# Performance work log

Hardware: AMD Instinct MI355X
Metric: run time of the kernel (lower is better)

## Reference

```python
import jax, jax.numpy as jnp
import numpy as np

# model dims
B, L, D, K = 4, 1024, 512, 24      # batch, seq_len, d_model, num_eigh
KU, KY, NL, DT = 3, 2, 4, 512      # ar depth u, ar depth y, num_layers, d_target
EPS = 1e-5


def _hankel_eigh():
    # Hankel matrix Z[i,j] = 2 / ((i+j)^3 - (i+j)), i,j in 1..L; top-K eigenpairs
    idx = np.arange(1, L + 1, dtype=np.float64)
    s = idx[:, None] + idx[None, :]
    Z = 2.0 / (s ** 3 - s)
    vals, vecs = np.linalg.eigh(Z)  # ascending
    return (jnp.asarray(vals[-K:], jnp.float32),       # [K]
            jnp.asarray(vecs[:, -K:], jnp.float32))    # [L, K]


def setup_inputs() -> dict:
    key = jax.random.key(0)
    ks = jax.random.split(key, 12)
    sc = 1.0 / np.sqrt(D)
    eig_vals, eig_vecs = _hankel_eigh()
    return {
        "inputs": jax.random.normal(ks[0], (B, L, D), jnp.float32),
        "emb_w": jax.random.normal(ks[1], (D, D), jnp.float32) * sc,
        "emb_b": jnp.zeros((D,), jnp.float32),
        "ln_scale": jnp.ones((NL, D), jnp.float32),
        "ln_bias": jnp.zeros((NL, D), jnp.float32),
        "m_y": jax.random.normal(ks[2], (NL, D, KY, D), jnp.float32) * 0.02,
        "m_u": jax.random.normal(ks[3], (NL, D, D, KU), jnp.float32) * sc,
        "m_phi": jax.random.normal(ks[4], (NL, D * K, D), jnp.float32) * 0.02,
        "w1": jax.random.normal(ks[5], (NL, D, 2 * D), jnp.float32) * sc,
        "b1": jnp.zeros((NL, 2 * D), jnp.float32),
        "proj_w": jax.random.normal(ks[6], (D, DT), jnp.float32) * sc,
        "proj_b": jnp.zeros((DT,), jnp.float32),
        "eig_vals": eig_vals,
        "eig_vecs": eig_vecs,
    }


def _layer_norm(x, s, b):
    mu = jnp.mean(x, axis=-1, keepdims=True)
    var = jnp.mean(jnp.square(x - mu), axis=-1, keepdims=True)
    return (x - mu) * jax.lax.rsqrt(var + EPS) * s + b


def _stu(x, m_y_l, m_u_l, m_phi_l, eig_vals, eig_vecs):
    # x: [B, L, D]
    n = 2 * L
    U = jnp.fft.rfft(x, n=n, axis=1)                 # [B, nf, D]
    V = jnp.fft.rfft(eig_vecs, n=n, axis=0)          # [nf, K]
    # causal conv of each eigvec filter with each channel -> x_tilde [B, L, K, D]
    xt = jnp.fft.irfft(U[:, :, None, :] * V[None, :, :, None], n=n, axis=1)[:, :L]
    xt = xt * (eig_vals[None, None, :, None] ** 0.25)
    delta_phi = xt.reshape(B, L, K * D) @ m_phi_l    # [B, L, D]
    ar = jnp.zeros_like(delta_phi)
    for i in range(KU):
        c = jnp.einsum('bli,oi->blo', x, m_u_l[:, :, i])
        if i > 0:
            c = jnp.pad(c, ((0, 0), (i, 0), (0, 0)))[:, :L]
        ar = ar + c
    deltas = delta_phi + ar
    # y_t = sum_{j<KY} m_y[:,j,:] @ y_{t-1-j} + delta_t  (sequential recurrence)
    def step(carry, d_t):                            # carry [B, KY, D], d_t [B, D]
        y = jnp.einsum('okd,bkd->bo', m_y_l, carry) + d_t
        carry = jnp.concatenate([y[:, None, :], carry[:, :-1]], axis=1)
        return carry, y
    _, ys = jax.lax.scan(step, jnp.zeros((B, KY, D), x.dtype),
                         jnp.transpose(deltas, (1, 0, 2)))
    return jnp.transpose(ys, (1, 0, 2))              # [B, L, D]


def reference(inputs, emb_w, emb_b, ln_scale, ln_bias, m_y, m_u, m_phi,
              w1, b1, proj_w, proj_b, eig_vals, eig_vecs):
    x = inputs @ emb_w + emb_b
    for l in range(NL):
        z = x
        h = _layer_norm(x, ln_scale[l], ln_bias[l])
        h = _stu(h, m_y[l], m_u[l], m_phi[l], eig_vals, eig_vecs)
        h = jax.nn.gelu(h, approximate=False)        # torch GELU default (erf)
        g = h @ w1[l] + b1[l]
        a, b = jnp.split(g, 2, axis=-1)
        h = a * jax.nn.sigmoid(b)                    # GLU(dim=-1)
        x = h + z                                    # residual (dropout=0, eval)
    return x @ proj_w + proj_b
```

## Files before the change

### kernel.cpp

```cpp
#include <hip/hip_runtime.h>
#include <math.h>

typedef __bf16 bf;
typedef __attribute__((ext_vector_type(4))) __bf16 bfv4;
typedef __attribute__((ext_vector_type(8))) __bf16 bfv8;
typedef __attribute__((ext_vector_type(4))) float f32x4;

__device__ __forceinline__ void gload16(const void* g, void* l) {
  __builtin_amdgcn_global_load_lds((const __attribute__((address_space(1))) void*)g,
                                   (__attribute__((address_space(3))) void*)l, 16, 0, 0);
}

struct GOp {
  const bf* A; long la, lKa, lMa, sAz; int zshA, kzA;
  const bf* B; long lb, lKb, sBz; int zmskB, kzB;
  float* C; long ldc, sCz;
  bf* Cb; long ldcb, sCbz;
  const float* bias; int K, maskCmp, mBlk;
};

template<int tB,int tF32,int tB16,int tMASK,int tACC>
__device__ __forceinline__ void gbody(const GOp g, int z, bf* lsA, bf* lsB, const bf* zpg) {
  const int t = threadIdx.x;
  const long m0 = (long)blockIdx.x * 128, n0 = (long)blockIdx.y * 128;
  const bf* Ap = g.A + (long)(z >> g.zshA) * g.sAz;
  const bf* Bp = g.B + (long)(z & g.zmskB) * g.sBz;
  const int w = t >> 6, l = t & 63;
  const int wm = (w >> 1) * 64, wn = (w & 1) * 64;
  const int lr = l & 15, lk = (l >> 4) * 8;
  const int r0 = t >> 2, ko = (t & 3) * 8;
  const long rowA1 = m0 + r0, rowA2 = rowA1 + 64;
  const long baseA1 = (rowA1 >> 9) * g.lMa + (rowA1 & 511) * g.la;
  const long baseA2 = (rowA2 >> 9) * g.lMa + (rowA2 & 511) * g.la;
  const long baseB1 = (n0 + r0) * g.lb;
  const int zbA = z * g.kzA, zbB = z * g.kzB;
  const int ct = ((int)rowA1 + 1) & 7;
  const long convB = (long)ct * 2065 + 1023 - (long)rowA1;
  f32x4 acc[4][4];
  #pragma unroll
  for (int i = 0; i < 4; i++)
    #pragma unroll
    for (int j = 0; j < 4; j++) acc[i][j] = (f32x4){0.f, 0.f, 0.f, 0.f};

  for (int k0 = 0; k0 < g.K; k0 += 32) {
    const int kk = k0 + ko;
    const int bA = (kk >> 9) + zbA, bB = (kk >> 9) + zbB;
    const long kb = (long)bB * g.lKb + (kk & 511);
    const bf* ga; const bf* ga2;
    if (tMASK == 3) {
      ga  = Ap + convB + kk;
      ga2 = ga - 64;
    } else {
      const long ka = (long)bA * g.lKa + (kk & 511);
      ga  = Ap + baseA1 + ka;
      ga2 = Ap + baseA2 + ka;
      if (tMASK == 1) { if ((int)(rowA1 & 15) < bA) { ga = zpg; ga2 = zpg; } }
      if (tMASK == 2) { if ((int)(rowA1 & 63) < g.maskCmp) { ga = zpg; ga2 = zpg; } }
    }
    const bf* gb = Bp + baseB1 + kb;
    gload16(ga,            &lsA[t * 8]);
    gload16(ga2,           &lsA[2048 + t * 8]);
    gload16(gb,            &lsB[t * 8]);
    gload16(gb + 64 * g.lb, &lsB[2048 + t * 8]);
    __syncthreads();
    bfv8 av[4], bv[4];
    #pragma unroll
    for (int i = 0; i < 4; i++) av[i] = *(const bfv8*)&lsA[(wm + i * 16 + lr) * 32 + lk];
    #pragma unroll
    for (int i = 0; i < 4; i++) bv[i] = *(const bfv8*)&lsB[(wn + i * 16 + lr) * 32 + lk];
    #pragma unroll
    for (int i = 0; i < 4; i++)
      #pragma unroll
      for (int j = 0; j < 4; j++)
        acc[i][j] = __builtin_amdgcn_mfma_f32_16x16x32_bf16(av[i], bv[j], acc[i][j], 0, 0, 0);
    __syncthreads();
  }
  const int orow = (l >> 4) * 4, ocol = lr;
  #pragma unroll
  for (int i = 0; i < 4; i++)
    #pragma unroll
    for (int j = 0; j < 4; j++) {
      long col = n0 + wn + j * 16 + ocol;
      float bb = tB ? g.bias[col] : 0.f;
      #pragma unroll
      for (int r = 0; r < 4; r++) {
        long row = m0 + wm + i * 16 + orow + r;
        float v = acc[i][j][r] + bb;
        if (tF32) {
          long idx = (long)z * g.sCz + row * g.ldc + col;
          if (tACC) v += g.C[idx];
          g.C[idx] = v;
        }
        if (tB16) g.Cb[(long)z * g.sCbz + row * g.ldcb + col] = (bf)v;
      }
    }
}

template<int tB,int tF32,int tB16,int tMASK,int tACC,int tSPEC,
         int sB,int sF32,int sB16,int sMASK,int sACC>
__global__ __launch_bounds__(256) void gemm_k(GOp g, GOp gx, const bf* __restrict__ zpg) {
  __shared__ bf lsA[4096], lsB[4096];
  int z = blockIdx.z;
  if (tSPEC && z == (int)gridDim.z - 1) {
    if ((int)blockIdx.x >= gx.mBlk) return;
    gbody<sB,sF32,sB16,sMASK,sACC>(gx, 0, lsA, lsB, zpg);
  } else {
    gbody<tB,tF32,tB16,tMASK,tACC>(g, z, lsA, lsB, zpg);
  }
}

static inline GOp mkop(const void* A, long la, long lKa, long lMa, long sAz, int zshA, int kzA,
                       const void* B, long lb, long lKb, long sBz, int zmskB, int kzB,
                       void* C, long ldc, long sCz, void* Cb, long ldcb, long sCbz,
                       const void* bias, int K, int maskCmp, int mBlk) {
  GOp g;
  g.A = (const bf*)A; g.la = la; g.lKa = lKa; g.lMa = lMa; g.sAz = sAz; g.zshA = zshA; g.kzA = kzA;
  g.B = (const bf*)B; g.lb = lb; g.lKb = lKb; g.sBz = sBz; g.zmskB = zmskB; g.kzB = kzB;
  g.C = (float*)C; g.ldc = ldc; g.sCz = sCz;
  g.Cb = (bf*)Cb; g.ldcb = ldcb; g.sCbz = sCbz;
  g.bias = (const float*)bias; g.K = K; g.maskCmp = maskCmp; g.mBlk = mBlk;
  return g;
}

template<int tB,int tF32,int tB16,int tMASK,int tACC,int tSPEC=0,
         int sB=0,int sF32=0,int sB16=0,int sMASK=0,int sACC=0>
static inline void LG(hipStream_t st, int gx, int gy, int gz, const GOp& g, const GOp& gs, const bf* zpg) {
  gemm_k<tB,tF32,tB16,tMASK,tACC,tSPEC,sB,sF32,sB16,sMASK,sACC>
      <<<dim3(gx, gy, gz), 256, 0, st>>>(g, gs, zpg);
}


template<typename TI, typename TO>
__global__ __launch_bounds__(256) void k_trt(const TI* __restrict__ in, TO* __restrict__ out,
                                             long ldin, long inz, long ldout, long outz) {
  __shared__ float tile[64][65];
  int z = blockIdx.z;
  int c0 = blockIdx.x * 64, r0 = blockIdx.y * 64;
  int tx = threadIdx.x & 63, ty = threadIdx.x >> 6;
  #pragma unroll
  for (int i = ty; i < 64; i += 4) tile[i][tx] = (float)in[(long)z * inz + (long)(c0 + i) * ldin + r0 + tx];
  __syncthreads();
  #pragma unroll
  for (int i = ty; i < 64; i += 4) out[(long)z * outz + (long)(r0 + i) * ldout + c0 + tx] = (TO)tile[tx][i];
}

__global__ __launch_bounds__(256) void k_trtS(const float* __restrict__ in, bf* __restrict__ out,
                                              long ldin, long ldout, const float* __restrict__ scl) {
  __shared__ float tile[64][65];
  int c0 = blockIdx.x * 64, r0 = blockIdx.y * 64;
  int tx = threadIdx.x & 63, ty = threadIdx.x >> 6;
  #pragma unroll
  for (int i = ty; i < 64; i += 4) tile[i][tx] = in[(long)(c0 + i) * ldin + r0 + tx];
  __syncthreads();
  float sc = scl[(c0 + tx) >> 9];
  #pragma unroll
  for (int i = ty; i < 64; i += 4) out[(long)(r0 + i) * ldout + c0 + tx] = (bf)(tile[tx][i] * sc);
}

__global__ void k_scl(const float* __restrict__ evals, float* __restrict__ scl) {
  int k = threadIdx.x;
  if (k < 24) scl[k] = powf(evals[k], 0.25f);
}

__global__ void k_pvec(const float* __restrict__ evecs, bf* __restrict__ out) {
  long id = (long)blockIdx.x * 256 + threadIdx.x;
  if (id >= 24L * 16512) return;
  int kf = (int)(id / 16512);
  int rem = (int)(id % 16512);
  int c = rem / 2064, j = rem % 2064;
  int d = j - c;
  float v = (d >= 0 && d <= 1023) ? evecs[(long)(1023 - d) * 24 + kf] : 0.f;
  out[id] = (bf)v;
}

__global__ void k_mut(const float* __restrict__ mul_, bf* __restrict__ out) {
  long id = (long)blockIdx.x * 256 + threadIdx.x;
  long r = id >> 9; int d = (int)(id & 511);
  int i = (int)(r >> 9), o = (int)(r & 511);
  out[id] = (bf)mul_[(long)o * 1536 + d * 3 + i];
}

__global__ void k_buildCM(const float* __restrict__ myl, bf* __restrict__ cmpow) {
  long id = (long)blockIdx.x * 256 + threadIdx.x;
  int half = (int)(id >> 20);
  int r = (int)(id & 1048575);
  int p = r >> 10, q = r & 1023;
  float v;
  if (half == 0) v = (p == q) ? 1.f : 0.f;
  else if (p < 512) v = myl[(long)p * 1024 + q];
  else v = (q == p - 512) ? 1.f : 0.f;
  cmpow[id] = (bf)v;
}

__global__ __launch_bounds__(256) void k_ln(const float* __restrict__ x, const float* __restrict__ sc,
                                            const float* __restrict__ bi, bf* __restrict__ hb) {
  __shared__ float red[8];
  long row = blockIdx.x;
  const float* xr = x + row * 512;
  int t = threadIdx.x;
  float a = xr[t], b2 = xr[t + 256];
  float s = a + b2;
  #pragma unroll
  for (int o = 32; o; o >>= 1) s += __shfl_down(s, o, 64);
  if ((t & 63) == 0) red[t >> 6] = s;
  __syncthreads();
  float mu = (red[0] + red[1] + red[2] + red[3]) * (1.f / 512.f);
  __syncthreads();
  float c1 = a - mu, c2 = b2 - mu;
  float qq = c1 * c1 + c2 * c2;
  #pragma unroll
  for (int o = 32; o; o >>= 1) qq += __shfl_down(qq, o, 64);
  if ((t & 63) == 0) red[t >> 6] = qq;
  __syncthreads();
  float var = (red[0] + red[1] + red[2] + red[3]) * (1.f / 512.f);
  float rs = rsqrtf(var + 1e-5f);
  hb[row * 512 + t]       = (bf)(c1 * rs * sc[t] + bi[t]);
  hb[row * 512 + t + 256] = (bf)(c2 * rs * sc[t + 256] + bi[t + 256]);
}

__global__ void k_deltasS(const float* __restrict__ dp, long stride, int S,
                          const bf* __restrict__ callb, bf* __restrict__ db) {
  long id = (long)blockIdx.x * 256 + threadIdx.x;
  int o = (int)(id & 511); long row = id >> 9; int tt = (int)(row & 1023);
  float v = 0.f;
  for (int zz = 0; zz < S; ++zz) v += dp[(long)zz * stride + id];
  for (int i = 0; i < 3; ++i)
    if (tt >= i) v += (float)callb[(row - i) * 1536 + i * 512 + o];
  db[id] = (bf)v;
}

__global__ void k_egather(const float* __restrict__ dp, long stride, int S,
                          float* __restrict__ E, bf* __restrict__ eb0) {
  long id = (long)blockIdx.x * 256 + threadIdx.x;
  int p = (int)(id & 1023); long r = id >> 10;
  int b = (int)(r >> 6), c = (int)(r & 63);
  int tq = c * 16 + ((p < 512) ? 15 : 14);
  long idx = ((long)(b << 10) + tq) * 512 + (p & 511);
  float v = 0.f;
  for (int zz = 0; zz < S; ++zz) v += dp[(long)zz * stride + idx];
  E[id] = v; eb0[id] = (bf)v;
}

__global__ void k_sfinal(const float* __restrict__ E, bf* __restrict__ ssb) {
  long id = (long)blockIdx.x * 256 + threadIdx.x;
  int c = (int)((id >> 10) & 63);
  ssb[id] = (c > 0) ? (bf)E[id - 1024] : (bf)0.f;
}

__global__ void k_combgelu(const float* __restrict__ dp, long stride, int S,
                           const bf* __restrict__ outh, bf* __restrict__ yg) {
  long id = (long)blockIdx.x * 256 + threadIdx.x;
  int o = (int)(id & 511); long row = id >> 9;
  int b = (int)(row >> 10), tt = (int)(row & 1023);
  int c = tt >> 4, j = tt & 15;
  long wv = ((long)(j * 512 + o)) * 256 + b * 64 + c;
  float v = (float)outh[wv];
  for (int zz = 0; zz < S; ++zz) v += dp[(long)zz * stride + id];
  yg[id] = (bf)(0.5f * v * (1.f + erff(v * 0.70710678118654752f)));
}

__global__ void k_glures(const bf* __restrict__ g, float* __restrict__ x) {
  long id = (long)blockIdx.x * 256 + threadIdx.x;
  int o = (int)(id & 511); long row = id >> 9;
  float a = (float)g[row * 1024 + o], bb = (float)g[row * 1024 + 512 + o];
  x[id] = x[id] + a / (1.f + expf(-bb));
}

__global__ void k_cast(const float* __restrict__ in, bf* __restrict__ out, long n4) {
  long id = (long)blockIdx.x * 256 + threadIdx.x;
  if (id >= n4) return;
  float4 v = *(const float4*)(in + id * 4);
  bfv4 o; o[0] = (bf)v.x; o[1] = (bf)v.y; o[2] = (bf)v.z; o[3] = (bf)v.w;
  *(bfv4*)(out + id * 4) = o;
}

__global__ void k_fill(float* p, long n, float v) {
  long id = (long)blockIdx.x * 256 + threadIdx.x;
  if (id < n) p[id] = v;
}

struct Lay {
  long ZPG, SCL, EMBT, PROJT, PVEC, CMPOW, CMT2, WU, X, MPHITL, MUTL, W1TL,
       HB, HTB, DSLOT, DP, RC, E, EB0, EB1, SSTB, need;
  int nk, S;
};
static Lay mkLay(int nk, int S) {
  Lay L; long o = 0;
  auto al = [&](long sz) { long r = o; o += (sz + 255) & ~255L; return r; };
  L.nk = nk; L.S = S;
  L.ZPG   = al(4096);
  L.SCL   = al(256);
  L.EMBT  = al(524288);
  L.PROJT = al(524288);
  L.PVEC  = al(24L * 16512 * 2);
  L.CMPOW = al(17L * 2097152);
  L.CMT2  = al(2L * 2097152);
  L.WU    = al(8388608);
  L.X     = al(8388608);
  L.MPHITL= al(12582912);
  L.MUTL  = al(1572864);
  L.W1TL  = al(1048576);
  L.HB    = al(4194304);
  L.HTB   = al(4194304);
  L.DSLOT = al(4194304);
  L.DP    = al((long)S * 8388608);
  long rc = (long)nk * 4194304;
  if (rc < 16777216) rc = 16777216;
  L.RC    = al(rc);
  L.E     = al(1048576);
  L.EB0   = al(524288);
  L.EB1   = al(524288);
  L.SSTB  = al(524288);
  L.need  = o;
  return L;
}

extern "C" void kernel_launch(void* const* d_in, const int* in_sizes, int n_in,
                              void* d_out, int out_size, void* d_ws, size_t ws_size,
                              hipStream_t stream) {
  Lay L = mkLay(12, 4);
  if (L.need > (long)ws_size) L = mkLay(8, 4);
  if (L.need > (long)ws_size) L = mkLay(4, 2);
  if (L.need > (long)ws_size) {
    k_fill<<<8192, 256, 0, stream>>>((float*)d_out, 2097152, 1.0e6f + (float)(ws_size >> 20));
    return;
  }
  const float* inp  = (const float*)d_in[0];
  const float* embw = (const float*)d_in[1];
  const float* embb = (const float*)d_in[2];
  const float* lns  = (const float*)d_in[3];
  const float* lnb  = (const float*)d_in[4];
  const float* m_y  = (const float*)d_in[5];
  const float* m_u  = (const float*)d_in[6];
  const float* mphi = (const float*)d_in[7];
  const float* w1   = (const float*)d_in[8];
  const float* b1   = (const float*)d_in[9];
  const float* pw   = (const float*)d_in[10];
  const float* pb   = (const float*)d_in[11];
  const float* evals = (const float*)d_in[12];
  const float* evecs = (const float*)d_in[13];

  char* w = (char*)d_ws;
  bf*    ZPG   = (bf*)(w + L.ZPG);
  float* SCL   = (float*)(w + L.SCL);
  bf*    EMBT  = (bf*)(w + L.EMBT);
  bf*    PROJT = (bf*)(w + L.PROJT);
  bf*    PVEC  = (bf*)(w + L.PVEC);
  bf*    CMPOW = (bf*)(w + L.CMPOW);
  bf*    CMT2a = (bf*)(w + L.CMT2);
  bf*    CMT2b = CMT2a + 1048576;
  bf*    WUa   = (bf*)(w + L.WU);
  bf*    WUb   = (bf*)(w + L.WU + 4194304);
  float* X     = (float*)(w + L.X);
  bf*    MPHITL= (bf*)(w + L.MPHITL);
  bf*    MUTL  = (bf*)(w + L.MUTL);
  bf*    W1TL  = (bf*)(w + L.W1TL);
  bf*    HB    = (bf*)(w + L.HB);
  bf*    HTB   = (bf*)(w + L.HTB);
  bf*    DELTAB= (bf*)(w + L.DSLOT);
  bf*    YGB   = (bf*)(w + L.DSLOT);
  float* DP    = (float*)(w + L.DP);
  bf*    XTC   = (bf*)(w + L.RC);
  bf*    CALLB = (bf*)(w + L.RC);
  bf*    OUTH  = (bf*)(w + L.RC + 12582912);
  bf*    G     = (bf*)(w + L.RC);
  float* E     = (float*)(w + L.E);
  bf*    EB0   = (bf*)(w + L.EB0);
  bf*    EB1   = (bf*)(w + L.EB1);
  bf*    SSTB  = (bf*)(w + L.SSTB);
  bf*    INB   = HB;
  hipStream_t st = stream;
  const int nk = L.nk, S = L.S, nchunk = 24 / nk;
  const long DPS = 2097152;
  const int Kcphi = nk * 512 / S, kzphi = Kcphi >> 9;
  const int Kcy = 8192 / S, kzy = Kcy >> 9;
  GOp gnull = {};

  hipMemsetAsync(w + L.ZPG, 0, 4096, st);

  k_scl<<<1, 32, 0, st>>>(evals, SCL);
  k_pvec<<<1549, 256, 0, st>>>(evecs, PVEC);
  k_trt<float, bf><<<dim3(8, 8, 1), 256, 0, st>>>(embw, EMBT, 512, 0, 512, 0);
  k_trt<float, bf><<<dim3(8, 8, 1), 256, 0, st>>>(pw, PROJT, 512, 0, 512, 0);
  k_cast<<<2048, 256, 0, st>>>(inp, INB, 524288);
  LG<1,1,0,0,0>(st, 32, 4, 1,
      mkop(INB, 512, 512, 262144, 0, 30, 0, EMBT, 512, 512, 0, 0, 0,
           X, 512, 0, nullptr, 0, 0, embb, 512, 0, 0), gnull, ZPG);

  for (int l = 0; l < 4; ++l) {
    k_buildCM<<<8192, 256, 0, st>>>(m_y + (long)l * 524288, CMPOW);
    k_trt<bf, bf><<<dim3(16, 16, 1), 256, 0, st>>>(CMPOW + 1048576, CMT2a, 1024, 0, 1024, 0);
    bf* curT = CMT2a;
    for (int r = 0; r < 4; ++r) {
      int s = 1 << r;
      bf* nxtT = (r & 1) ? CMT2a : CMT2b;
      GOp mn = mkop(CMPOW + 1048576, 1024, 512, 524288, 1048576, 0, 0,
                    curT, 1024, 512, 0, 0, 0,
                    nullptr, 0, 0, CMPOW + (long)(s + 1) * 1048576, 1024, 1048576,
                    nullptr, 1024, 0, 0);
      GOp sp = mkop(curT, 1024, 512, 524288, 0, 30, 0,
                    CMPOW + (long)s * 1048576, 1024, 512, 0, 0, 0,
                    nullptr, 0, 0, nxtT, 1024, 0,
                    nullptr, 1024, 0, 8);
      LG<0,0,1,0,0, 1, 0,0,1,0,0>(st, 8, 8, s + 1, mn, sp, ZPG);
      curT = nxtT;
    }
    k_trtS<<<dim3(192, 8, 1), 256, 0, st>>>(mphi + (long)l * 6291456, MPHITL, 512, 12288, SCL);
    k_mut<<<3072, 256, 0, st>>>(m_u + (long)l * 786432, MUTL);
    k_trt<float, bf><<<dim3(8, 16, 1), 256, 0, st>>>(w1 + (long)l * 524288, W1TL, 1024, 0, 512, 0);

    k_ln<<<4096, 256, 0, st>>>(X, lns + l * 512, lnb + l * 512, HB);
    k_trt<bf, bf><<<dim3(16, 8, 4), 256, 0, st>>>(HB, HTB, 512, 524288, 1024, 524288);

    for (int kc = 0; kc < nchunk; ++kc) {
      LG<0,0,1,3,0>(st, 8, 4, 4 * nk,
          mkop(PVEC + (long)kc * nk * 16512, 0, 0, 0, 16512, 2, 0,
               HTB, 1024, 512, 524288, 3, 0,
               nullptr, 0, 0, XTC, 512, 524288, nullptr, 1024, 0, 0), gnull, ZPG);
      GOp pg = mkop(XTC, 512, 2097152, 262144, 0, 30, kzphi,
                    MPHITL + (long)kc * nk * 512, 12288, 512, 0, 0, kzphi,
                    DP, 512, DPS, nullptr, 0, 0, nullptr, Kcphi, 0, 0);
      if (kc == 0) LG<0,1,0,0,0>(st, 32, 4, S, pg, gnull, ZPG);
      else         LG<0,1,0,0,1>(st, 32, 4, S, pg, gnull, ZPG);
    }

    LG<0,0,1,0,0>(st, 32, 12, 1,
        mkop(HB, 512, 512, 262144, 0, 30, 0, MUTL, 512, 512, 0, 0, 0,
             nullptr, 0, 0, CALLB, 1536, 0, nullptr, 512, 0, 0), gnull, ZPG);
    k_deltasS<<<8192, 256, 0, st>>>(DP, DPS, S, CALLB, DELTAB);

    LG<0,1,0,1,0>(st, 32, 4, S,
        mkop(DELTAB, 512, -512, 262144, 0, 30, kzy,
             CMPOW, 1024, 1048576, 0, 0, kzy,
             DP, 512, DPS, nullptr, 0, 0, nullptr, Kcy, 0, 0), gnull, ZPG);

    k_egather<<<1024, 256, 0, st>>>(DP, DPS, S, E, EB0);
    const bf* Wc = CMPOW + 16L * 1048576;
    const bf* Uc = curT;
    bf* EBc = EB0; bf* EBn = EB1;
    bf* WUn = WUa;
    for (int k = 1; k <= 5; ++k) {
      int sh = 1 << (k - 1);
      GOp mn = mkop(Wc, 1024, 512, 524288, (long)(Uc - Wc), 0, 0,
                    Uc, 1024, 512, (long)(Wc - Uc), 1, 0,
                    nullptr, 0, 0, WUn, 1024, 1048576, nullptr, 1024, 0, 0);
      GOp sp = mkop(EBc - (long)sh * 1024, 1024, 512, 524288, 0, 30, 0,
                    Wc, 1024, 512, 0, 0, 0,
                    E, 1024, 0, EBn, 1024, 0, nullptr, 1024, sh, 2);
      LG<0,0,1,0,0, 1, 0,1,1,2,1>(st, 8, 8, 3, mn, sp, ZPG);
      Wc = WUn; Uc = WUn + 1048576;
      WUn = (k & 1) ? WUb : WUa;
      bf* tmp = EBc; EBc = EBn; EBn = tmp;
    }
    LG<0,1,0,2,1>(st, 2, 8, 1,
        mkop(EBc - 32L * 1024, 1024, 512, 524288, 0, 30, 0,
             Wc, 1024, 512, 0, 0, 0,
             E, 1024, 0, nullptr, 0, 0, nullptr, 1024, 32, 0), gnull, ZPG);
    k_sfinal<<<1024, 256, 0, st>>>(E, SSTB);

    LG<0,0,1,0,0>(st, 64, 2, 1,
        mkop(CMPOW + 1048576, 1024, 512, 1048576, 0, 30, 0,
             SSTB, 1024, 512, 0, 0, 0,
             nullptr, 0, 0, OUTH, 256, 0, nullptr, 1024, 0, 0), gnull, ZPG);
    k_combgelu<<<8192, 256, 0, st>>>(DP, DPS, S, OUTH, YGB);
    LG<1,0,1,0,0>(st, 32, 8, 1,
        mkop(YGB, 512, 512, 262144, 0, 30, 0, W1TL, 512, 512, 0, 0, 0,
             nullptr, 0, 0, G, 1024, 0, b1 + (long)l * 1024, 512, 0, 0), gnull, ZPG);
    k_glures<<<8192, 256, 0, st>>>(G, X);
  }

  k_cast<<<2048, 256, 0, st>>>(X, INB, 524288);
  LG<1,1,0,0,0>(st, 32, 4, 1,
      mkop(INB, 512, 512, 262144, 0, 30, 0, PROJT, 512, 512, 0, 0, 0,
           (float*)d_out, 512, 0, nullptr, 0, 0, pb, 512, 0, 0), gnull, ZPG);
}
```

Baseline: 3.136 ms.

## Fold companion-matrix power rounds into conv and phi GEMM launches as extra blocks

The four repeated-squaring rounds that build the powers of the AR-y companion matrix no longer run as standalone launches. Each round is appended as extra z-slices to a convolution or phi GEMM launch in the first chunk iterations, with the tile work flattened across blocks and split between a power-product op and a transpose-update op. The initial matrix build and its transpose are merged into one prep kernel that also writes the identity half of the transposed buffer. The aim is to cut launch count and fill idle compute units behind the small power GEMMs. The risk is that the power rounds now depend on enough chunk iterations existing, and that the extra blocks can lengthen the tail of the host GEMMs.

```diff
diff --git a/kernel.cpp b/kernel.cpp
--- a/kernel.cpp
+++ b/kernel.cpp
@@ -16,13 +16,13 @@
   const bf* B; long lb, lKb, sBz; int zmskB, kzB;
   float* C; long ldc, sCz;
   bf* Cb; long ldcb, sCbz;
-  const float* bias; int K, maskCmp, mBlk;
+  const float* bias; int K, maskCmp, mBlk, spS;
 };
 
 template<int tB,int tF32,int tB16,int tMASK,int tACC>
-__device__ __forceinline__ void gbody(const GOp g, int z, bf* lsA, bf* lsB, const bf* zpg) {
+__device__ __forceinline__ void gbody(const GOp g, int z, long m0, long n0,
+                                      bf* lsA, bf* lsB, const bf* zpg) {
   const int t = threadIdx.x;
-  const long m0 = (long)blockIdx.x * 128, n0 = (long)blockIdx.y * 128;
   const bf* Ap = g.A + (long)(z >> g.zshA) * g.sAz;
   const bf* Bp = g.B + (long)(z & g.zmskB) * g.sBz;
   const int w = t >> 6, l = t & 63;
@@ -58,9 +58,9 @@
       if (tMASK == 2) { if ((int)(rowA1 & 63) < g.maskCmp) { ga = zpg; ga2 = zpg; } }
     }
     const bf* gb = Bp + baseB1 + kb;
-    gload16(ga,            &lsA[t * 8]);
-    gload16(ga2,           &lsA[2048 + t * 8]);
-    gload16(gb,            &lsB[t * 8]);
+    gload16(ga,             &lsA[t * 8]);
+    gload16(ga2,            &lsA[2048 + t * 8]);
+    gload16(gb,             &lsB[t * 8]);
     gload16(gb + 64 * g.lb, &lsB[2048 + t * 8]);
     __syncthreads();
     bfv8 av[4], bv[4];
@@ -96,37 +96,45 @@
     }
 }
 
-template<int tB,int tF32,int tB16,int tMASK,int tACC,int tSPEC,
-         int sB,int sF32,int sB16,int sMASK,int sACC>
-__global__ __launch_bounds__(256) void gemm_k(GOp g, GOp gx, const bf* __restrict__ zpg) {
+template<int tB,int tF32,int tB16,int tMASK,int tACC,int tSPEC=0,
+         int sB=0,int sF32=0,int sB16=0,int sMASK=0,int sACC=0>
+__global__ __launch_bounds__(256) void gemm_k(GOp g, GOp gx, GOp gy, int Zmain,
+                                              const bf* __restrict__ zpg) {
   __shared__ bf lsA[4096], lsB[4096];
   int z = blockIdx.z;
-  if (tSPEC && z == (int)gridDim.z - 1) {
-    if ((int)blockIdx.x >= gx.mBlk) return;
-    gbody<sB,sF32,sB16,sMASK,sACC>(gx, 0, lsA, lsB, zpg);
+  if (tSPEC && z >= Zmain) {
+    int flat = (z - Zmain) * (int)(gridDim.x * gridDim.y)
+             + (int)blockIdx.y * (int)gridDim.x + (int)blockIdx.x;
+    if (flat >= gx.mBlk) return;
+    int zz = flat >> 6, t64 = flat & 63;
+    long m0 = (long)(t64 >> 3) * 128, n0 = (long)(t64 & 7) * 128;
+    if (zz < gx.spS) gbody<sB,sF32,sB16,sMASK,sACC>(gx, zz, m0, n0, lsA, lsB, zpg);
+    else             gbody<sB,sF32,sB16,sMASK,sACC>(gy, 0,  m0, n0, lsA, lsB, zpg);
   } else {
-    gbody<tB,tF32,tB16,tMASK,tACC>(g, z, lsA, lsB, zpg);
+    gbody<tB,tF32,tB16,tMASK,tACC>(g, z, (long)blockIdx.x * 128, (long)blockIdx.y * 128,
+                                   lsA, lsB, zpg);
   }
 }
 
 static inline GOp mkop(const void* A, long la, long lKa, long lMa, long sAz, int zshA, int kzA,
                        const void* B, long lb, long lKb, long sBz, int zmskB, int kzB,
                        void* C, long ldc, long sCz, void* Cb, long ldcb, long sCbz,
-                       const void* bias, int K, int maskCmp, int mBlk) {
+                       const void* bias, int K) {
   GOp g;
   g.A = (const bf*)A; g.la = la; g.lKa = lKa; g.lMa = lMa; g.sAz = sAz; g.zshA = zshA; g.kzA = kzA;
   g.B = (const bf*)B; g.lb = lb; g.lKb = lKb; g.sBz = sBz; g.zmskB = zmskB; g.kzB = kzB;
   g.C = (float*)C; g.ldc = ldc; g.sCz = sCz;
   g.Cb = (bf*)Cb; g.ldcb = ldcb; g.sCbz = sCbz;
-  g.bias = (const float*)bias; g.K = K; g.maskCmp = maskCmp; g.mBlk = mBlk;
+  g.bias = (const float*)bias; g.K = K; g.maskCmp = 0; g.mBlk = 0; g.spS = 0;
   return g;
 }
 
 template<int tB,int tF32,int tB16,int tMASK,int tACC,int tSPEC=0,
          int sB=0,int sF32=0,int sB16=0,int sMASK=0,int sACC=0>
-static inline void LG(hipStream_t st, int gx, int gy, int gz, const GOp& g, const GOp& gs, const bf* zpg) {
+static inline void LG(hipStream_t st, int gx_, int gy_, int gz_, const GOp& g,
+                      const GOp& gsx, const GOp& gsy, int Zmain, const bf* zpg) {
   gemm_k<tB,tF32,tB16,tMASK,tACC,tSPEC,sB,sF32,sB16,sMASK,sACC>
-      <<<dim3(gx, gy, gz), 256, 0, st>>>(g, gs, zpg);
+      <<<dim3(gx_, gy_, gz_), 256, 0, st>>>(g, gsx, gsy, Zmain, zpg);
 }
 
 
@@ -180,16 +188,38 @@
   out[id] = (bf)mul_[(long)o * 1536 + d * 3 + i];
 }
 
-__global__ void k_buildCM(const float* __restrict__ myl, bf* __restrict__ cmpow) {
-  long id = (long)blockIdx.x * 256 + threadIdx.x;
-  int half = (int)(id >> 20);
-  int r = (int)(id & 1048575);
-  int p = r >> 10, q = r & 1023;
-  float v;
-  if (half == 0) v = (p == q) ? 1.f : 0.f;
-  else if (p < 512) v = myl[(long)p * 1024 + q];
-  else v = (q == p - 512) ? 1.f : 0.f;
-  cmpow[id] = (bf)v;
+__global__ __launch_bounds__(256) void k_prep(const float* __restrict__ myl,
+                                              bf* __restrict__ cmpow, bf* __restrict__ trs) {
+  __shared__ float t[64][65];
+  long bid = blockIdx.x;
+  if (bid < 10240) {
+    long id = bid * 256 + threadIdx.x;
+    if (id < 2097152) {
+      int half = (int)(id >> 20);
+      int r = (int)(id & 1048575);
+      int p = r >> 10, q = r & 1023;
+      float v;
+      if (half == 0) v = (p == q) ? 1.f : 0.f;
+      else if (p < 512) v = myl[(long)p * 1024 + q];
+      else v = (q == p - 512) ? 1.f : 0.f;
+      cmpow[id] = (bf)v;
+    } else if (id < 2621440) {
+      long id2 = id - 2097152;
+      int x = (int)(id2 >> 9), y = (int)(id2 & 511);
+      trs[(long)x * 1024 + 512 + y] = (bf)((x == y) ? 1.f : 0.f);
+    }
+  } else {
+    int tile = (int)(bid - 10240);
+    int txx = tile >> 3, tyy = tile & 7;
+    int lx = threadIdx.x & 63, ly = threadIdx.x >> 6;
+    #pragma unroll
+    for (int i = ly; i < 64; i += 4)
+      t[i][lx] = myl[(long)(tyy * 64 + i) * 1024 + txx * 64 + lx];
+    __syncthreads();
+    #pragma unroll
+    for (int i = ly; i < 64; i += 4)
+      trs[(long)(txx * 64 + i) * 1024 + tyy * 64 + lx] = (bf)t[lx][i];
+  }
 }
 
 __global__ __launch_bounds__(256) void k_ln(const float* __restrict__ x, const float* __restrict__ sc,
@@ -280,8 +310,8 @@
 }
 
 struct Lay {
-  long ZPG, SCL, EMBT, PROJT, PVEC, CMPOW, CMT2, WU, X, MPHITL, MUTL, W1TL,
-       HB, HTB, DSLOT, DP, RC, E, EB0, EB1, SSTB, need;
+  long ZPG, SSTB, SCL, EMBT, PROJT, PVEC, CMPOW, TRS, WU, X, MPHITL, MUTL, W1TL,
+       HB, HTB, DSLOT, DP, RC, E, EB0, EB1, need;
   int nk, S;
 };
 static Lay mkLay(int nk, int S) {
@@ -289,12 +319,13 @@
   auto al = [&](long sz) { long r = o; o += (sz + 255) & ~255L; return r; };
   L.nk = nk; L.S = S;
   L.ZPG   = al(4096);
+  L.SSTB  = al(524288);
   L.SCL   = al(256);
   L.EMBT  = al(524288);
   L.PROJT = al(524288);
   L.PVEC  = al(24L * 16512 * 2);
   L.CMPOW = al(17L * 2097152);
-  L.CMT2  = al(2L * 2097152);
+  L.TRS   = al(2L * 2097152);
   L.WU    = al(8388608);
   L.X     = al(8388608);
   L.MPHITL= al(12582912);
@@ -310,7 +341,6 @@
   L.E     = al(1048576);
   L.EB0   = al(524288);
   L.EB1   = al(524288);
-  L.SSTB  = al(524288);
   L.need  = o;
   return L;
 }
@@ -342,13 +372,14 @@
 
   char* w = (char*)d_ws;
   bf*    ZPG   = (bf*)(w + L.ZPG);
+  bf*    SSTB  = (bf*)(w + L.SSTB);
   float* SCL   = (float*)(w + L.SCL);
   bf*    EMBT  = (bf*)(w + L.EMBT);
   bf*    PROJT = (bf*)(w + L.PROJT);
   bf*    PVEC  = (bf*)(w + L.PVEC);
   bf*    CMPOW = (bf*)(w + L.CMPOW);
-  bf*    CMT2a = (bf*)(w + L.CMT2);
-  bf*    CMT2b = CMT2a + 1048576;
+  bf*    TRSa  = (bf*)(w + L.TRS);
+  bf*    TRSb  = TRSa + 1048576;
   bf*    WUa   = (bf*)(w + L.WU);
   bf*    WUb   = (bf*)(w + L.WU + 4194304);
   float* X     = (float*)(w + L.X);
@@ -367,7 +398,6 @@
   float* E     = (float*)(w + L.E);
   bf*    EB0   = (bf*)(w + L.EB0);
   bf*    EB1   = (bf*)(w + L.EB1);
-  bf*    SSTB  = (bf*)(w + L.SSTB);
   bf*    INB   = HB;
   hipStream_t st = stream;
   const int nk = L.nk, S = L.S, nchunk = 24 / nk;
@@ -375,6 +405,7 @@
   const int Kcphi = nk * 512 / S, kzphi = Kcphi >> 9;
   const int Kcy = 8192 / S, kzy = Kcy >> 9;
   GOp gnull = {};
+  const int BIGZ = 1 << 30;
 
   hipMemsetAsync(w + L.ZPG, 0, 4096, st);
 
@@ -385,26 +416,10 @@
   k_cast<<<2048, 256, 0, st>>>(inp, INB, 524288);
   LG<1,1,0,0,0>(st, 32, 4, 1,
       mkop(INB, 512, 512, 262144, 0, 30, 0, EMBT, 512, 512, 0, 0, 0,
-           X, 512, 0, nullptr, 0, 0, embb, 512, 0, 0), gnull, ZPG);
+           X, 512, 0, nullptr, 0, 0, embb, 512), gnull, gnull, BIGZ, ZPG);
 
   for (int l = 0; l < 4; ++l) {
-    k_buildCM<<<8192, 256, 0, st>>>(m_y + (long)l * 524288, CMPOW);
-    k_trt<bf, bf><<<dim3(16, 16, 1), 256, 0, st>>>(CMPOW + 1048576, CMT2a, 1024, 0, 1024, 0);
-    bf* curT = CMT2a;
-    for (int r = 0; r < 4; ++r) {
-      int s = 1 << r;
-      bf* nxtT = (r & 1) ? CMT2a : CMT2b;
-      GOp mn = mkop(CMPOW + 1048576, 1024, 512, 524288, 1048576, 0, 0,
-                    curT, 1024, 512, 0, 0, 0,
-                    nullptr, 0, 0, CMPOW + (long)(s + 1) * 1048576, 1024, 1048576,
-                    nullptr, 1024, 0, 0);
-      GOp sp = mkop(curT, 1024, 512, 524288, 0, 30, 0,
-                    CMPOW + (long)s * 1048576, 1024, 512, 0, 0, 0,
-                    nullptr, 0, 0, nxtT, 1024, 0,
-                    nullptr, 1024, 0, 8);
-      LG<0,0,1,0,0, 1, 0,0,1,0,0>(st, 8, 8, s + 1, mn, sp, ZPG);
-      curT = nxtT;
-    }
+    k_prep<<<10368, 256, 0, st>>>(m_y + (long)l * 524288, CMPOW, TRSa);
     k_trtS<<<dim3(192, 8, 1), 256, 0, st>>>(mphi + (long)l * 6291456, MPHITL, 512, 12288, SCL);
     k_mut<<<3072, 256, 0, st>>>(m_u + (long)l * 786432, MUTL);
     k_trt<float, bf><<<dim3(8, 16, 1), 256, 0, st>>>(w1 + (long)l * 524288, W1TL, 1024, 0, 512, 0);
@@ -412,65 +427,103 @@
     k_ln<<<4096, 256, 0, st>>>(X, lns + l * 512, lnb + l * 512, HB);
     k_trt<bf, bf><<<dim3(16, 8, 4), 256, 0, st>>>(HB, HTB, 512, 524288, 1024, 524288);
 
+    int hostRound = 0;
     for (int kc = 0; kc < nchunk; ++kc) {
-      LG<0,0,1,3,0>(st, 8, 4, 4 * nk,
-          mkop(PVEC + (long)kc * nk * 16512, 0, 0, 0, 16512, 2, 0,
-               HTB, 1024, 512, 524288, 3, 0,
-               nullptr, 0, 0, XTC, 512, 524288, nullptr, 1024, 0, 0), gnull, ZPG);
-      GOp pg = mkop(XTC, 512, 2097152, 262144, 0, 30, kzphi,
-                    MPHITL + (long)kc * nk * 512, 12288, 512, 0, 0, kzphi,
-                    DP, 512, DPS, nullptr, 0, 0, nullptr, Kcphi, 0, 0);
-      if (kc == 0) LG<0,1,0,0,0>(st, 32, 4, S, pg, gnull, ZPG);
-      else         LG<0,1,0,0,1>(st, 32, 4, S, pg, gnull, ZPG);
+      GOp gconv = mkop(PVEC + (long)kc * nk * 16512, 0, 0, 0, 16512, 2, 0,
+                       HTB, 1024, 512, 524288, 3, 0,
+                       nullptr, 0, 0, XTC, 512, 524288, nullptr, 1024);
+      if (hostRound < 4) {
+        int s = 1 << hostRound;
+        bf* TRScur = (hostRound & 1) ? TRSb : TRSa;
+        bf* TRSnxt = (hostRound & 1) ? TRSa : TRSb;
+        GOp dx = mkop(CMPOW + 1048576, 1024, 512, 524288, 1048576, 0, 0,
+                      TRScur, 1024, 512, 0, 0, 0,
+                      nullptr, 0, 0, CMPOW + (long)(s + 1) * 1048576, 1024, 1048576,
+                      nullptr, 1024);
+        dx.mBlk = 64 * (s + 1); dx.spS = s;
+        GOp dy = mkop(TRScur, 1024, 512, 524288, 0, 0, 0,
+                      CMPOW + (long)s * 1048576, 1024, 512, 0, 0, 0,
+                      nullptr, 0, 0, TRSnxt, 1024, 0, nullptr, 1024);
+        int nzs = (64 * (s + 1) + 31) / 32;
+        LG<0,0,1,3,0, 1, 0,0,1,0,0>(st, 8, 4, 4 * nk + nzs, gconv, dx, dy, 4 * nk, ZPG);
+        ++hostRound;
+      } else {
+        LG<0,0,1,3,0>(st, 8, 4, 4 * nk, gconv, gnull, gnull, BIGZ, ZPG);
+      }
+      GOp gphi = mkop(XTC, 512, 2097152, 262144, 0, 30, kzphi,
+                      MPHITL + (long)kc * nk * 512, 12288, 512, 0, 0, kzphi,
+                      DP, 512, DPS, nullptr, 0, 0, nullptr, Kcphi);
+      if (hostRound < 4) {
+        int s = 1 << hostRound;
+        bf* TRScur = (hostRound & 1) ? TRSb : TRSa;
+        bf* TRSnxt = (hostRound & 1) ? TRSa : TRSb;
+        GOp dx = mkop(CMPOW + 1048576, 1024, 512, 524288, 1048576, 0, 0,
+                      TRScur, 1024, 512, 0, 0, 0,
+                      nullptr, 0, 0, CMPOW + (long)(s + 1) * 1048576, 1024, 1048576,
+                      nullptr, 1024);
+        dx.mBlk = 64 * (s + 1); dx.spS = s;
+        GOp dy = mkop(TRScur, 1024, 512, 524288, 0, 0, 0,
+                      CMPOW + (long)s * 1048576, 1024, 512, 0, 0, 0,
+                      nullptr, 0, 0, TRSnxt, 1024, 0, nullptr, 1024);
+        int nzs = (64 * (s + 1) + 127) / 128;
+        if (kc == 0) LG<0,1,0,0,0, 1, 0,0,1,0,0>(st, 32, 4, S + nzs, gphi, dx, dy, S, ZPG);
+        else         LG<0,1,0,0,1, 1, 0,0,1,0,0>(st, 32, 4, S + nzs, gphi, dx, dy, S, ZPG);
+        ++hostRound;
+      } else {
+        if (kc == 0) LG<0,1,0,0,0>(st, 32, 4, S, gphi, gnull, gnull, BIGZ, ZPG);
+        else         LG<0,1,0,0,1>(st, 32, 4, S, gphi, gnull, gnull, BIGZ, ZPG);
+      }
     }
 
     LG<0,0,1,0,0>(st, 32, 12, 1,
         mkop(HB, 512, 512, 262144, 0, 30, 0, MUTL, 512, 512, 0, 0, 0,
-             nullptr, 0, 0, CALLB, 1536, 0, nullptr, 512, 0, 0), gnull, ZPG);
+             nullptr, 0, 0, CALLB, 1536, 0, nullptr, 512), gnull, gnull, BIGZ, ZPG);
     k_deltasS<<<8192, 256, 0, st>>>(DP, DPS, S, CALLB, DELTAB);
 
     LG<0,1,0,1,0>(st, 32, 4, S,
         mkop(DELTAB, 512, -512, 262144, 0, 30, kzy,
              CMPOW, 1024, 1048576, 0, 0, kzy,
-             DP, 512, DPS, nullptr, 0, 0, nullptr, Kcy, 0, 0), gnull, ZPG);
+             DP, 512, DPS, nullptr, 0, 0, nullptr, Kcy), gnull, gnull, BIGZ, ZPG);
 
     k_egather<<<1024, 256, 0, st>>>(DP, DPS, S, E, EB0);
     const bf* Wc = CMPOW + 16L * 1048576;
-    const bf* Uc = curT;
+    const bf* Uc = TRSa;
     bf* EBc = EB0; bf* EBn = EB1;
     bf* WUn = WUa;
     for (int k = 1; k <= 5; ++k) {
       int sh = 1 << (k - 1);
       GOp mn = mkop(Wc, 1024, 512, 524288, (long)(Uc - Wc), 0, 0,
                     Uc, 1024, 512, (long)(Wc - Uc), 1, 0,
-                    nullptr, 0, 0, WUn, 1024, 1048576, nullptr, 1024, 0, 0);
+                    nullptr, 0, 0, WUn, 1024, 1048576, nullptr, 1024);
       GOp sp = mkop(EBc - (long)sh * 1024, 1024, 512, 524288, 0, 30, 0,
                     Wc, 1024, 512, 0, 0, 0,
-                    E, 1024, 0, EBn, 1024, 0, nullptr, 1024, sh, 2);
-      LG<0,0,1,0,0, 1, 0,1,1,2,1>(st, 8, 8, 3, mn, sp, ZPG);
+                    E, 1024, 0, EBn, 1024, 0, nullptr, 1024);
+      sp.maskCmp = sh; sp.mBlk = 16; sp.spS = 99;
+      LG<0,0,1,0,0, 1, 0,1,1,2,1>(st, 8, 8, 3, mn, sp, gnull, 2, ZPG);
       Wc = WUn; Uc = WUn + 1048576;
       WUn = (k & 1) ? WUb : WUa;
       bf* tmp = EBc; EBc = EBn; EBn = tmp;
     }
-    LG<0,1,0,2,1>(st, 2, 8, 1,
-        mkop(EBc - 32L * 1024, 1024, 512, 524288, 0, 30, 0,
-             Wc, 1024, 512, 0, 0, 0,
-             E, 1024, 0, nullptr, 0, 0, nullptr, 1024, 32, 0), gnull, ZPG);
+    GOp fe = mkop(EBc - 32L * 1024, 1024, 512, 524288, 0, 30, 0,
+                  Wc, 1024, 512, 0, 0, 0,
+                  E, 1024, 0, nullptr, 0, 0, nullptr, 1024);
+    fe.maskCmp = 32;
+    LG<0,1,0,2,1>(st, 2, 8, 1, fe, gnull, gnull, BIGZ, ZPG);
     k_sfinal<<<1024, 256, 0, st>>>(E, SSTB);
 
     LG<0,0,1,0,0>(st, 64, 2, 1,
         mkop(CMPOW + 1048576, 1024, 512, 1048576, 0, 30, 0,
              SSTB, 1024, 512, 0, 0, 0,
-             nullptr, 0, 0, OUTH, 256, 0, nullptr, 1024, 0, 0), gnull, ZPG);
+             nullptr, 0, 0, OUTH, 256, 0, nullptr, 1024), gnull, gnull, BIGZ, ZPG);
     k_combgelu<<<8192, 256, 0, st>>>(DP, DPS, S, OUTH, YGB);
     LG<1,0,1,0,0>(st, 32, 8, 1,
         mkop(YGB, 512, 512, 262144, 0, 30, 0, W1TL, 512, 512, 0, 0, 0,
-             nullptr, 0, 0, G, 1024, 0, b1 + (long)l * 1024, 512, 0, 0), gnull, ZPG);
+             nullptr, 0, 0, G, 1024, 0, b1 + (long)l * 1024, 512), gnull, gnull, BIGZ, ZPG);
     k_glures<<<8192, 256, 0, st>>>(G, X);
   }
 
   k_cast<<<2048, 256, 0, st>>>(X, INB, 524288);
   LG<1,1,0,0,0>(st, 32, 4, 1,
       mkop(INB, 512, 512, 262144, 0, 30, 0, PROJT, 512, 512, 0, 0, 0,
-           (float*)d_out, 512, 0, nullptr, 0, 0, pb, 512, 0, 0), gnull, ZPG);
-}
+           (float*)d_out, 512, 0, nullptr, 0, 0, pb, 512), gnull, gnull, BIGZ, ZPG);
+}
```

Measured after the change: 2.986 ms. 1.05x faster.
